# Performance work log

Hardware: AMD Instinct MI355X
Metric: run time of the kernel (lower is better)

## Reference

```python
import jax, jax.numpy as jnp
import numpy as np

B, T, V, H, E, MAX_OOV = 128, 200, 50257, 256, 128, 50


def setup_inputs() -> dict:
    key = jax.random.key(0)
    ks = jax.random.split(key, 17)
    s = 0.05  # param scale
    return {
        "decoder_input": jax.random.randint(ks[0], (B, 1), 0, V),
        "encoder_outputs": jax.random.normal(ks[1], (B, T, 2 * H), jnp.float32),
        "encoder_idxs": jax.random.randint(ks[2], (B, T), 0, V),
        "prev_state": jax.random.normal(ks[3], (1, B, H), jnp.float32),
        "selective_read": jax.random.normal(ks[4], (B, 1, 2 * H), jnp.float32) * s,
        "step": 1,
        "emb": jax.random.normal(ks[5], (V, E), jnp.float32) * s,
        "W_ih": jax.random.normal(ks[6], (3 * H, E + 2 * H), jnp.float32) * s,
        "W_hh": jax.random.normal(ks[7], (3 * H, H), jnp.float32) * s,
        "b_ih": jax.random.normal(ks[8], (3 * H,), jnp.float32) * s,
        "b_hh": jax.random.normal(ks[9], (3 * H,), jnp.float32) * s,
        "Wi_w": jax.random.normal(ks[10], (H, 2 * H), jnp.float32) * s,
        "Wi_b": jax.random.normal(ks[11], (H,), jnp.float32) * s,
        "Wg_w": jax.random.normal(ks[12], (V, H), jnp.float32) * s,
        "Wg_b": jax.random.normal(ks[13], (V,), jnp.float32) * s,
        "Wc_w": jax.random.normal(ks[14], (H, 2 * H), jnp.float32) * s,
        "Wc_b": jax.random.normal(ks[15], (H,), jnp.float32) * s,
    }


def _gru_cell(x, h, W_ih, W_hh, b_ih, b_hh):
    # torch GRUCell math, gate order r,z,n
    gi = x @ W_ih.T + b_ih
    gh = h @ W_hh.T + b_hh
    i_r, i_z, i_n = jnp.split(gi, 3, axis=-1)
    h_r, h_z, h_n = jnp.split(gh, 3, axis=-1)
    r = jax.nn.sigmoid(i_r + h_r)
    z = jax.nn.sigmoid(i_z + h_z)
    n = jnp.tanh(i_n + r * h_n)
    return (1.0 - z) * n + z * h


def reference(decoder_input, encoder_outputs, encoder_idxs, prev_state, selective_read,
              step, emb, W_ih, W_hh, b_ih, b_hh, Wi_w, Wi_b, Wg_w, Wg_b, Wc_w, Wc_b):
    dtype = encoder_outputs.dtype
    if step == 0:
        prev_state = (encoder_outputs[:, -1] @ Wi_w.T + Wi_b)[None]      # 1,B,H
        selective_read = jnp.zeros((B, 1, 2 * H), dtype)
    embedded = emb[decoder_input[:, 0]]                                   # B,E
    gru_in = jnp.concatenate([selective_read[:, 0], embedded], axis=-1)   # B,2H+E
    decode_hidden = _gru_cell(gru_in, prev_state[0], W_ih, W_hh, b_ih, b_hh)  # B,H

    score_g = decode_hidden @ Wg_w.T + Wg_b                               # B,V
    enc_proj = jnp.tanh(jnp.einsum('bte,he->bth', encoder_outputs, Wc_w) + Wc_b)  # B,T,H
    score_c = jnp.tanh(jnp.einsum('bth,bh->bt', enc_proj, decode_hidden))         # B,T
    score_c = score_c + jnp.where(encoder_idxs == 0, -10000.0, 0.0).astype(dtype)

    probs = jax.nn.softmax(jnp.concatenate([score_g, score_c], axis=1), axis=1)   # B,V+T
    prob_g, prob_c = probs[:, :V], probs[:, V:]
    prob_g = jnp.concatenate([prob_g, jnp.full((B, MAX_OOV), 1e-4, dtype)], axis=1)  # B,V+oov

    # copy-distribution aggregation: scatter-add prob_c by vocab id (replaces one-hot bmm)
    prob_c_to_g = jnp.zeros((B, V + MAX_OOV), dtype).at[
        jnp.arange(B)[:, None], encoder_idxs].add(prob_c)
    prob_out = (prob_c_to_g + prob_g)[:, None, :]                          # B,1,V+oov

    # selective read for next step
    match = (encoder_idxs == decoder_input).astype(dtype)                  # B,T
    tot = match.sum(axis=1, keepdims=True)
    match = jnp.where(tot > 1, match / tot, match)
    prob_appeared = prob_c * match
    selective_read_new = jnp.einsum('bt,bte->be', prob_appeared, encoder_outputs)[:, None, :]  # B,1,2H
    return prob_out, decode_hidden, selective_read_new
```

## Files before the change

### kernel.cpp

```cpp
#include <hip/hip_runtime.h>

typedef __bf16 bf16;
typedef __bf16 bf16x4 __attribute__((ext_vector_type(4)));
typedef __bf16 bf16x8 __attribute__((ext_vector_type(8)));
typedef float f32x4 __attribute__((ext_vector_type(4)));

#define B_ 128
#define T_ 200
#define V_ 50257
#define H_ 256
#define E_ 128
#define OOV_ 50
#define VO_ 50307
#define NRG 64
#define NTS 4
#define GSC 786
#define NROWP 50304
#define PSTR 800
#define PBSTR 50368
#define GPJ 400
#define GWPACK 12576

__device__ __forceinline__ float sigmoid_(float x) { return 1.0f / (1.0f + __expf(-x)); }
__device__ __forceinline__ float tanh_(float x) { return 1.0f - 2.0f / (__expf(2.0f * x) + 1.0f); }

__global__ void k_front(const float* Wc_w, bf16* WcPack,
                        const int* step_p, const float* enc, const float* prev,
                        const float* selread, const int* dec, const float* emb,
                        const float* Wi_w, const float* Wi_b,
                        float* hT, float* ginT,
                        const float* Wg_w, bf16* WgPack) {
    if (blockIdx.x < 128) {
        int gid = blockIdx.x * 256 + threadIdx.x;
        int n = gid >> 7;
        int k = (gid & 127) * 4;
        float4 v = *(const float4*)(Wc_w + n * 512 + k);
        int kstep = k >> 5, kin = k & 31;
        int q = kin >> 3, j0 = kin & 7;
        int r = n & 15, nt = n >> 4;
        int lane = q * 16 + r;
        bf16* d = WcPack + (((nt * 16 + kstep) * 64) + lane) * 8 + j0;
        d[0] = (bf16)v.x; d[1] = (bf16)v.y; d[2] = (bf16)v.z; d[3] = (bf16)v.w;
    } else if (blockIdx.x < 256) {
        int b = blockIdx.x - 128, t = threadIdx.x;
        int step = step_p[0];
        float h;
        if (step == 0) {
            float acc = Wi_b[t];
            const float* er = enc + (b * T_ + (T_ - 1)) * 512;
            const float* wr = Wi_w + t * 512;
            for (int k = 0; k < 512; ++k) acc += er[k] * wr[k];
            h = acc;
        } else {
            h = prev[b * H_ + t];
        }
        hT[t * B_ + b] = h;
        for (int k = t; k < 512; k += 256)
            ginT[k * B_ + b] = (step == 0) ? 0.0f : selread[b * 512 + k];
        if (t < E_)
            ginT[(512 + t) * B_ + b] = emb[dec[b] * E_ + t];
    } else {
        int gid = (blockIdx.x - 256) * 256 + threadIdx.x;
        int row = gid >> 6;
        int k = (gid & 63) * 4;
        float4 v = (row < V_) ? *(const float4*)(Wg_w + row * 256 + k)
                              : float4{0.f, 0.f, 0.f, 0.f};
        int nt = row >> 4, r = row & 15;
        int ks = k >> 5, kin = k & 31;
        int q = kin >> 3, j0 = kin & 7;
        int lane = q * 16 + r;
        bf16* d = WgPack + (((nt * 8 + ks) * 64) + lane) * 8 + j0;
        d[0] = (bf16)v.x; d[1] = (bf16)v.y; d[2] = (bf16)v.z; d[3] = (bf16)v.w;
    }
}

__global__ void k_gemm_gru(const float* W_ih, const float* b_ih,
                           const float* W_hh, const float* b_hh,
                           const float* ginT, const float* hT,
                           float* giT, float* ghT) {
    __shared__ float red[256];
    int rrow = blockIdx.x;
    int t = threadIdx.x;
    int b = t & 127, kh = t >> 7;
    const float* w = W_ih + rrow * 640 + kh * 320;
    const float* g = ginT + (kh * 320) * B_ + b;
    float a0 = 0.f, a1 = 0.f, a2 = 0.f, a3 = 0.f;
#pragma unroll 4
    for (int k = 0; k < 320; k += 4) {
        a0 += w[k]     * g[k * B_];
        a1 += w[k + 1] * g[(k + 1) * B_];
        a2 += w[k + 2] * g[(k + 2) * B_];
        a3 += w[k + 3] * g[(k + 3) * B_];
    }
    const float* w2 = W_hh + rrow * 256 + kh * 128;
    const float* hh = hT + (kh * 128) * B_ + b;
    float c0 = 0.f, c1 = 0.f, c2 = 0.f, c3 = 0.f;
#pragma unroll 4
    for (int k = 0; k < 128; k += 4) {
        c0 += w2[k]     * hh[k * B_];
        c1 += w2[k + 1] * hh[(k + 1) * B_];
        c2 += w2[k + 2] * hh[(k + 2) * B_];
        c3 += w2[k + 3] * hh[(k + 3) * B_];
    }
    red[t] = ((a0 + a1) + (a2 + a3));
    __syncthreads();
    if (kh == 0) giT[rrow * B_ + b] = b_ih[rrow] + red[b] + red[b + 128];
    __syncthreads();
    red[t] = ((c0 + c1) + (c2 + c3));
    __syncthreads();
    if (kh == 0) ghT[rrow * B_ + b] = b_hh[rrow] + red[b] + red[b + 128];
}

__global__ void k_gru_cell(const float* giT, const float* ghT, const float* hT,
                           float* out_dh, bf16* Apack) {
    int b = blockIdx.x, j = threadIdx.x;
    float ir = giT[j * B_ + b], iz = giT[(256 + j) * B_ + b], in_ = giT[(512 + j) * B_ + b];
    float hr = ghT[j * B_ + b], hz = ghT[(256 + j) * B_ + b], hn = ghT[(512 + j) * B_ + b];
    float hp = hT[j * B_ + b];
    float r = sigmoid_(ir + hr);
    float z = sigmoid_(iz + hz);
    float n = tanh_(in_ + r * hn);
    float h = (1.0f - z) * n + z * hp;
    out_dh[b * H_ + j] = h;
    int mt = b >> 4, rr = b & 15, ks = j >> 5, q = (j >> 3) & 3, jj = j & 7;
    Apack[(((mt * 8 + ks) * 64) + (q * 16 + rr)) * 8 + jj] = (bf16)h;
}

__global__ __launch_bounds__(512, 2) void k_score(const bf16* Apack, const bf16* WgPack,
                                                  const float* Wg_b,
                                                  bf16* expg, float* pg_part) {
    int tid = threadIdx.x;
    int w = tid >> 6, lane = tid & 63;
    int r = lane & 15, q = lane >> 4;
    int blk = blockIdx.x;
    int n0 = blk * NRG;
    const bf16* bbase = WgPack + (size_t)(blk * NTS * 8) * 512 + lane * 8;
    const bf16* abase = Apack + (w * 8) * 512 + lane * 8;
    f32x4 acc[NTS];
#pragma unroll
    for (int i = 0; i < NTS; ++i) acc[i] = (f32x4){0.f, 0.f, 0.f, 0.f};
#pragma unroll
    for (int ks = 0; ks < 8; ++ks) {
        bf16x8 a = *(const bf16x8*)(abase + ks * 512);
#pragma unroll
        for (int nt = 0; nt < NTS; ++nt) {
            bf16x8 bfr = *(const bf16x8*)(bbase + (nt * 8 + ks) * 512);
            acc[nt] = __builtin_amdgcn_mfma_f32_16x16x32_bf16(a, bfr, acc[nt], 0, 0, 0);
        }
    }
    float rsum[4] = {0.f, 0.f, 0.f, 0.f};
#pragma unroll
    for (int nt = 0; nt < NTS; ++nt) {
        int n = n0 + nt * 16 + r;
        bool valid = (n < V_);
        float wgb = Wg_b[valid ? n : (V_ - 1)];
#pragma unroll
        for (int rg = 0; rg < 4; ++rg) {
            int row = w * 16 + q * 4 + rg;
            float e = valid ? __expf(acc[nt][rg] + wgb) : 0.0f;
            rsum[rg] += e;
            expg[row * PBSTR + n] = (bf16)e;
        }
    }
#pragma unroll
    for (int rg = 0; rg < 4; ++rg) {
        float s = rsum[rg];
        s += __shfl_xor(s, 1);
        s += __shfl_xor(s, 2);
        s += __shfl_xor(s, 4);
        s += __shfl_xor(s, 8);
        if (r == 0) {
            int row = w * 16 + q * 4 + rg;
            pg_part[row * PSTR + blk] = s;
        }
    }
}

__global__ __launch_bounds__(256, 4) void k_proj(const float* enc, const bf16* WcPack,
                                                 const float* Wc_b, const float* dh,
                                                 const int* idxs, float* expc) {
    __shared__ unsigned char smem[34816];
    int tid = threadIdx.x;
    int w = tid >> 6, lane = tid & 63;
    int r = lane & 15, q = lane >> 4;
    int m0 = blockIdx.x * 64;
    bf16* As = (bf16*)smem;
    float* sred = (float*)(smem + 33792);
    f32x4 acc[16];
#pragma unroll
    for (int i = 0; i < 16; ++i) acc[i] = (f32x4){0.f, 0.f, 0.f, 0.f};
    for (int half = 0; half < 2; ++half) {
        __syncthreads();
#pragma unroll
        for (int ph = 0; ph < 2; ++ph) {
            float4 tmp[8];
#pragma unroll
            for (int j = 0; j < 8; ++j) {
                int f = (ph * 8 + j) * 256 + tid;
                int row = f >> 6, c4 = f & 63;
                tmp[j] = *(const float4*)(enc + (m0 + row) * 512 + half * 256 + c4 * 4);
            }
#pragma unroll
            for (int j = 0; j < 8; ++j) {
                int f = (ph * 8 + j) * 256 + tid;
                int row = f >> 6, c4 = f & 63;
                bf16x4 o;
                o[0] = (bf16)tmp[j].x; o[1] = (bf16)tmp[j].y;
                o[2] = (bf16)tmp[j].z; o[3] = (bf16)tmp[j].w;
                *(bf16x4*)(As + row * 264 + c4 * 4) = o;
            }
        }
        __syncthreads();
#pragma unroll
        for (int ks = 0; ks < 8; ++ks) {
            int kstep = half * 8 + ks;
            bf16x8 bfr[4];
#pragma unroll
            for (int ntl = 0; ntl < 4; ++ntl)
                bfr[ntl] = *(const bf16x8*)(WcPack + (((w * 4 + ntl) * 16 + kstep) * 64 + lane) * 8);
#pragma unroll
            for (int mt = 0; mt < 4; ++mt) {
                bf16x8 a = *(const bf16x8*)(As + (mt * 16 + r) * 264 + ks * 32 + q * 8);
#pragma unroll
                for (int ntl = 0; ntl < 4; ++ntl)
                    acc[mt * 4 + ntl] = __builtin_amdgcn_mfma_f32_16x16x32_bf16(a, bfr[ntl], acc[mt * 4 + ntl], 0, 0, 0);
            }
        }
    }
#pragma unroll
    for (int mt = 0; mt < 4; ++mt) {
#pragma unroll
        for (int rg = 0; rg < 4; ++rg) {
            int rowl = mt * 16 + q * 4 + rg;
            int row = m0 + rowl;
            int b = row / T_;
            float s = 0.0f;
#pragma unroll
            for (int ntl = 0; ntl < 4; ++ntl) {
                int n = (w * 4 + ntl) * 16 + r;
                float pv = tanh_(acc[mt * 4 + ntl][rg] + Wc_b[n]);
                s += pv * dh[b * H_ + n];
            }
            s += __shfl_xor(s, 1);
            s += __shfl_xor(s, 2);
            s += __shfl_xor(s, 4);
            s += __shfl_xor(s, 8);
            if (r == 0) sred[rowl * 4 + w] = s;
        }
    }
    __syncthreads();
    if (tid < 64) {
        float s = sred[tid * 4] + sred[tid * 4 + 1] + sred[tid * 4 + 2] + sred[tid * 4 + 3];
        int row = m0 + tid;
        int b = row / T_, t = row - b * T_;
        float sc = tanh_(s);
        if (idxs[b * T_ + t] == 0) sc -= 10000.0f;
        expc[row] = __expf(sc);
    }
}

__global__ void k_finish(const float* pg_part, const float* expc_, const int* idxs,
                         const int* dec, const float* enc, const bf16* expg,
                         float* out_prob, float* out_sel) {
    __shared__ float red[256];
    __shared__ float cf[256];
    int b = blockIdx.x >> 1, hf = blockIdx.x & 1;
    int t = threadIdx.x;
    float s = 0.0f;
    for (int i = t; i < GSC; i += 256) s += pg_part[b * PSTR + i];
    if (t < T_) s += expc_[b * T_ + t];
    red[t] = s;
    __syncthreads();
    for (int k = 128; k > 0; k >>= 1) {
        if (t < k) red[t] += red[t + k];
        __syncthreads();
    }
    float iv = 1.0f / red[0];
    __syncthreads();
    int d = dec[b];
    float ec = 0.0f;
    int ix = -1;
    int m = 0;
    if (t < T_) {
        ix = idxs[b * T_ + t];
        ec = expc_[b * T_ + t];
        m = (ix == d) ? 1 : 0;
    }
    cf[t] = m ? ec * iv : 0.0f;
    red[t] = m ? 1.0f : 0.0f;
    __syncthreads();
    for (int k = 128; k > 0; k >>= 1) {
        if (t < k) red[t] += red[t + k];
        __syncthreads();
    }
    float tot = red[0];
    float scale = (tot > 1.0f) ? 1.0f / tot : 1.0f;
    int dim = t + hf * 256;
    float a0 = 0.0f;
    for (int tt = 0; tt < T_; ++tt) {
        float c = cf[tt];
        if (c != 0.0f) a0 += c * scale * enc[(b * T_ + tt) * 512 + dim];
    }
    out_sel[b * 512 + dim] = a0;
    const int halfc = (VO_ + 1) / 2;
    int cl0 = hf * halfc;
    int cl1 = (cl0 + halfc < VO_) ? cl0 + halfc : VO_;
    int base = b * VO_;
    const bf16* eg = expg + b * PBSTR;
    int c0a = (cl0 + 3) & ~3;
    int c1a = cl1 & ~3;
    if (t < c0a - cl0) {
        int col = cl0 + t;
        out_prob[base + col] = (col < V_) ? (float)eg[col] * iv : 1e-4f;
    }
    if (t < cl1 - c1a) {
        int col = c1a + t;
        out_prob[base + col] = (col < V_) ? (float)eg[col] * iv : 1e-4f;
    }
    for (int col = c0a + t * 4; col < c1a; col += 256 * 4) {
        bf16x4 ev = *(const bf16x4*)(eg + col);
#pragma unroll
        for (int c = 0; c < 4; ++c) {
            int cc = col + c;
            out_prob[base + cc] = (cc < V_) ? (float)ev[c] * iv : 1e-4f;
        }
    }
    __threadfence();
    __syncthreads();
    if (t < T_ && ix >= cl0 && ix < cl1)
        atomicAdd(&out_prob[base + ix], ec * iv);
}

extern "C" void kernel_launch(void* const* d_in, const int* in_sizes, int n_in,
                              void* d_out, int out_size, void* d_ws, size_t ws_size,
                              hipStream_t stream) {
    const int*   dec     = (const int*)d_in[0];
    const float* enc     = (const float*)d_in[1];
    const int*   idxs    = (const int*)d_in[2];
    const float* prev    = (const float*)d_in[3];
    const float* selread = (const float*)d_in[4];
    const int*   step_p  = (const int*)d_in[5];
    const float* emb     = (const float*)d_in[6];
    const float* W_ih    = (const float*)d_in[7];
    const float* W_hh    = (const float*)d_in[8];
    const float* b_ih    = (const float*)d_in[9];
    const float* b_hh    = (const float*)d_in[10];
    const float* Wi_w    = (const float*)d_in[11];
    const float* Wi_b    = (const float*)d_in[12];
    const float* Wg_w    = (const float*)d_in[13];
    const float* Wg_b    = (const float*)d_in[14];
    const float* Wc_w    = (const float*)d_in[15];
    const float* Wc_b    = (const float*)d_in[16];

    float* ws     = (float*)d_ws;
    float* hT     = ws;
    float* ginT   = ws + 32768;
    float* giT    = ws + 114688;
    float* ghT    = ws + 212992;
    float* expc   = ws + 311552;
    float* pgp    = ws + 337152;
    bf16*  Apack  = (bf16*)(ws + 741376);
    bf16*  WcPack = (bf16*)(ws + 757760);
    bf16*  expg   = (bf16*)(ws + 823296);

    float* out      = (float*)d_out;
    float* out_prob = out;
    float* out_dh   = out + 6439296;
    float* out_sel  = out + 6439296 + 32768;
    bf16*  WgPack   = (bf16*)out;

    k_front<<<256 + GWPACK, 256, 0, stream>>>(Wc_w, WcPack, step_p, enc, prev, selread,
                                              dec, emb, Wi_w, Wi_b, hT, ginT,
                                              Wg_w, WgPack);
    k_gemm_gru<<<768, 256, 0, stream>>>(W_ih, b_ih, W_hh, b_hh, ginT, hT, giT, ghT);
    k_gru_cell<<<B_, 256, 0, stream>>>(giT, ghT, hT, out_dh, Apack);
    k_proj<<<GPJ, 256, 0, stream>>>(enc, WcPack, Wc_b, out_dh, idxs, expc);
    k_score<<<GSC, 512, 0, stream>>>(Apack, WgPack, Wg_b, expg, pgp);
    k_finish<<<256, 256, 0, stream>>>(pgp, expc, idxs, dec, enc, expg, out_prob, out_sel);
}
```

Measured before the change: 311.2 us.

## Split finish kernel into reduce, wide normalize-write, and scatter kernels

The single finish kernel used 256 blocks, each normalizing half a batch row of the vocab output with scalar stores. It is replaced by three kernels: one computes the softmax denominator and the selective read per batch row, one normalizes the 6.4M-element output across 4096 blocks using aligned float4 stores, and one applies the copy-probability atomics. The aim is to spread the memory-bound output write over many more blocks and vectorize the stores. The cost is two extra kernel launches and an extra round trip through global memory for the inverse denominators.

```diff
diff --git a/kernel.cpp b/kernel.cpp
--- a/kernel.cpp
+++ b/kernel.cpp
@@ -259,13 +259,12 @@
     }
 }
 
-__global__ void k_finish(const float* pg_part, const float* expc_, const int* idxs,
-                         const int* dec, const float* enc, const bf16* expg,
-                         float* out_prob, float* out_sel) {
+__global__ void k_reduce(const float* pg_part, const float* expc_, const int* idxs,
+                         const int* dec, const float* enc, float* inv_out,
+                         float* out_sel) {
     __shared__ float red[256];
     __shared__ float cf[256];
-    int b = blockIdx.x >> 1, hf = blockIdx.x & 1;
-    int t = threadIdx.x;
+    int b = blockIdx.x, t = threadIdx.x;
     float s = 0.0f;
     for (int i = t; i < GSC; i += 256) s += pg_part[b * PSTR + i];
     if (t < T_) s += expc_[b * T_ + t];
@@ -276,13 +275,13 @@
         __syncthreads();
     }
     float iv = 1.0f / red[0];
+    if (t == 0) inv_out[b] = iv;
     __syncthreads();
     int d = dec[b];
     float ec = 0.0f;
-    int ix = -1;
     int m = 0;
     if (t < T_) {
-        ix = idxs[b * T_ + t];
+        int ix = idxs[b * T_ + t];
         ec = expc_[b * T_ + t];
         m = (ix == d) ? 1 : 0;
     }
@@ -295,40 +294,71 @@
     }
     float tot = red[0];
     float scale = (tot > 1.0f) ? 1.0f / tot : 1.0f;
-    int dim = t + hf * 256;
-    float a0 = 0.0f;
+    float a0 = 0.0f, a1 = 0.0f;
     for (int tt = 0; tt < T_; ++tt) {
         float c = cf[tt];
-        if (c != 0.0f) a0 += c * scale * enc[(b * T_ + tt) * 512 + dim];
-    }
-    out_sel[b * 512 + dim] = a0;
-    const int halfc = (VO_ + 1) / 2;
-    int cl0 = hf * halfc;
-    int cl1 = (cl0 + halfc < VO_) ? cl0 + halfc : VO_;
+        if (c != 0.0f) {
+            float wgt = c * scale;
+            a0 += wgt * enc[(b * T_ + tt) * 512 + t];
+            a1 += wgt * enc[(b * T_ + tt) * 512 + t + 256];
+        }
+    }
+    out_sel[b * 512 + t] = a0;
+    out_sel[b * 512 + t + 256] = a1;
+}
+
+__global__ __launch_bounds__(256) void k_normwrite(const bf16* expg, const float* inv,
+                                                   float* out_prob) {
+    int b = blockIdx.x >> 5, c = blockIdx.x & 31;
+    int t = threadIdx.x;
+    float iv = inv[b];
     int base = b * VO_;
     const bf16* eg = expg + b * PBSTR;
-    int c0a = (cl0 + 3) & ~3;
-    int c1a = cl1 & ~3;
-    if (t < c0a - cl0) {
-        int col = cl0 + t;
+    int i4s = (base + 3) >> 2;
+    int i4e = (base + VO_) >> 2;
+    int head = (i4s << 2) - base;
+    if (c == 0 && t < head) {
+        int col = t;
+        out_prob[base + col] = (float)eg[col] * iv;
+    }
+    int tail = (base + VO_) - (i4e << 2);
+    if (c == 31 && t < tail) {
+        int col = (i4e << 2) - base + t;
         out_prob[base + col] = (col < V_) ? (float)eg[col] * iv : 1e-4f;
     }
-    if (t < cl1 - c1a) {
-        int col = c1a + t;
-        out_prob[base + col] = (col < V_) ? (float)eg[col] * iv : 1e-4f;
-    }
-    for (int col = c0a + t * 4; col < c1a; col += 256 * 4) {
-        bf16x4 ev = *(const bf16x4*)(eg + col);
-#pragma unroll
-        for (int c = 0; c < 4; ++c) {
-            int cc = col + c;
-            out_prob[base + cc] = (cc < V_) ? (float)ev[c] * iv : 1e-4f;
-        }
-    }
-    __threadfence();
-    __syncthreads();
-    if (t < T_ && ix >= cl0 && ix < cl1)
-        atomicAdd(&out_prob[base + ix], ec * iv);
+    int n4 = i4e - i4s;
+    int per = (n4 + 31) >> 5;
+    int s0 = i4s + c * per;
+    int e0 = s0 + per; if (e0 > i4e) e0 = i4e;
+    int sh = ((i4s << 2) - base) == 0 ? 0 : (4 - ((base) & 3)) & 3;
+    sh = (4 - (base & 3)) & 3;
+    for (int i4 = s0 + t; i4 < e0; i4 += 256) {
+        int col = (i4 << 2) - base;
+        int al = col & ~3;
+        bf16x4 L0 = *(const bf16x4*)(eg + al);
+        bf16x4 L1 = *(const bf16x4*)(eg + al + 4);
+        float f0 = (float)L0[0], f1 = (float)L0[1], f2 = (float)L0[2], f3 = (float)L0[3];
+        float f4 = (float)L1[0], f5 = (float)L1[1], f6 = (float)L1[2], f7 = (float)L1[3];
+        float v0, v1, v2, v3;
+        if (sh == 0)      { v0 = f0; v1 = f1; v2 = f2; v3 = f3; }
+        else if (sh == 1) { v0 = f1; v1 = f2; v2 = f3; v3 = f4; }
+        else if (sh == 2) { v0 = f2; v1 = f3; v2 = f4; v3 = f5; }
+        else              { v0 = f3; v1 = f4; v2 = f5; v3 = f6; }
+        float o0 = (col + 0 < V_) ? v0 * iv : 1e-4f;
+        float o1 = (col + 1 < V_) ? v1 * iv : 1e-4f;
+        float o2 = (col + 2 < V_) ? v2 * iv : 1e-4f;
+        float o3 = (col + 3 < V_) ? v3 * iv : 1e-4f;
+        *(float4*)(out_prob + (i4 << 2)) = make_float4(o0, o1, o2, o3);
+    }
+}
+
+__global__ void k_scatter(const float* expc_, const int* idxs, const float* inv,
+                          float* out_prob) {
+    int b = blockIdx.x, t = threadIdx.x;
+    if (t < T_) {
+        int ix = idxs[b * T_ + t];
+        atomicAdd(&out_prob[b * VO_ + ix], expc_[b * T_ + t] * inv[b]);
+    }
 }
 
 extern "C" void kernel_launch(void* const* d_in, const int* in_sizes, int n_in,
@@ -357,6 +387,7 @@
     float* ginT   = ws + 32768;
     float* giT    = ws + 114688;
     float* ghT    = ws + 212992;
+    float* inv    = ws + 311296;
     float* expc   = ws + 311552;
     float* pgp    = ws + 337152;
     bf16*  Apack  = (bf16*)(ws + 741376);
@@ -376,5 +407,7 @@
     k_gru_cell<<<B_, 256, 0, stream>>>(giT, ghT, hT, out_dh, Apack);
     k_proj<<<GPJ, 256, 0, stream>>>(enc, WcPack, Wc_b, out_dh, idxs, expc);
     k_score<<<GSC, 512, 0, stream>>>(Apack, WgPack, Wg_b, expg, pgp);
-    k_finish<<<256, 256, 0, stream>>>(pgp, expc, idxs, dec, enc, expg, out_prob, out_sel);
-}
+    k_reduce<<<B_, 256, 0, stream>>>(pgp, expc, idxs, dec, enc, inv, out_sel);
+    k_normwrite<<<B_ * 32, 256, 0, stream>>>(expg, inv, out_prob);
+    k_scatter<<<B_, 256, 0, stream>>>(expc, idxs, inv, out_prob);
+}
```

Result: faster. 283.5 us (-8.9%).
